# Optimization experiments

Hardware: AMD Instinct MI355X
Metric: run time of the kernel (lower is better)

## Reference

```python
import jax, jax.numpy as jnp
import numpy as np

N = 196608   # total bonds in batch
H = 256      # hidden_size
NH = 8       # num_heads
D = H // NH  # att_size = 32
S = 4096     # num molecules (segments)
EPS = 1e-5


def setup_inputs() -> dict:
    key = jax.random.key(0)
    ks = jax.random.split(key, 12)
    f32 = jnp.float32
    return {
        "message": jax.random.normal(ks[0], (N, H), f32),
        "W_q": jax.random.normal(ks[1], (H, H), f32) * 0.05,
        "W_k": jax.random.normal(ks[2], (H, H), f32) * 0.05,
        "W_v": jax.random.normal(ks[3], (H, H), f32) * 0.05,
        "W_r": jax.random.normal(ks[4], (D, D), f32) * 0.15,
        "w_alpha": jax.random.normal(ks[5], (D,), f32),
        "w_beta": jax.random.normal(ks[6], (D,), f32),
        "W_o": jax.random.normal(ks[7], (H, H), f32) * 0.05,
        "b_o": jax.random.normal(ks[8], (H,), f32) * 0.02,
        "gamma": 1.0 + 0.1 * jax.random.normal(ks[9], (H,), f32),
        "beta_ln": 0.1 * jax.random.normal(ks[10], (H,), f32),
        "segment_ids": jnp.sort(jax.random.randint(ks[11], (N,), 0, S, dtype=jnp.int32)),
        "num_segments": S,
    }


def reference(message, W_q, W_k, W_v, W_r, w_alpha, w_beta, W_o, b_o,
              gamma, beta_ln, segment_ids, num_segments):
    scale = D ** (-0.5)
    # projections (torch Linear: y = x @ W.T), split heads -> [N, NH, D]
    q = (message @ W_q.T).reshape(-1, NH, D)
    k = (message @ W_k.T).reshape(-1, NH, D)
    v = (message @ W_v.T).reshape(-1, NH, D)
    # additive attention: softmax over feature dim d (per bond, per head)
    alpha = jax.nn.softmax(q * w_alpha * scale, axis=-1)
    # global query: sum over bonds within each molecule -> [S, NH, D]
    gq = jax.ops.segment_sum(alpha * q, segment_ids, num_segments=num_segments)
    p = gq[segment_ids] * k                      # [N, NH, D]
    beta = jax.nn.softmax(p * w_beta * scale, axis=-1)
    gk = jax.ops.segment_sum(beta * p, segment_ids, num_segments=num_segments)
    kvi = gk[segment_ids] * v                    # key-value interaction [N, NH, D]
    out = jnp.einsum('nhd,ed->nhe', kvi, W_r) + q  # weight_r on d, residual with q
    out = jax.nn.relu(out)                       # chemprop ReLU activation; dropout p=0
    out = out.reshape(-1, NH * D)
    out = out @ W_o.T + b_o
    # LayerNorm over hidden dim
    mu = jnp.mean(out, axis=-1, keepdims=True)
    var = jnp.mean(jnp.square(out - mu), axis=-1, keepdims=True)
    out = (out - mu) * jax.lax.rsqrt(var + EPS) * gamma + beta_ln
    # prepend cached zero vector (padding row), as the torch loop does for i == 0
    zero = jnp.zeros((1, H), dtype=out.dtype)
    return jnp.concatenate([zero, out], axis=0)
```

## Files before the change

### kernel.cpp

```cpp
#include <hip/hip_runtime.h>
#include <hip/hip_bf16.h>

#define N_BONDS 196608
#define HID     256
#define NSEG    4096
#define SMSCALE 0.17677669529663687f
#define LN_EPS  1e-5f
#define CHUNK   64

typedef __hip_bfloat16 bf16;
typedef __attribute__((ext_vector_type(8))) short short8_t;
typedef __attribute__((ext_vector_type(4))) float f32x4_t;

__device__ __forceinline__ float bf2f(bf16 x) { return __bfloat162float(x); }
__device__ __forceinline__ short f2bs(float f) {
    union { bf16 b; short s; } cv; cv.b = __float2bfloat16(f); return cv.s;
}
__device__ __forceinline__ float us2f(ushort u) {
    union { ushort u; bf16 b; } cv; cv.u = u; return __bfloat162float(cv.b);
}

__device__ __forceinline__ float gmax32(float x) {
#pragma unroll
    for (int m = 16; m >= 1; m >>= 1) x = fmaxf(x, __shfl_xor(x, m));
    return x;
}
__device__ __forceinline__ float gsum32(float x) {
#pragma unroll
    for (int m = 16; m >= 1; m >>= 1) x += __shfl_xor(x, m);
    return x;
}

__global__ void cast_kernel(const float* __restrict__ src, ushort* __restrict__ dst, int n4) {
    int i = blockIdx.x * blockDim.x + threadIdx.x;
    const int stride = gridDim.x * blockDim.x;
    for (; i < n4; i += stride) {
        float4 v = reinterpret_cast<const float4*>(src)[i];
        union { ushort4 u; bf16 b[4]; } cv;
        cv.b[0] = __float2bfloat16(v.x);
        cv.b[1] = __float2bfloat16(v.y);
        cv.b[2] = __float2bfloat16(v.z);
        cv.b[3] = __float2bfloat16(v.w);
        reinterpret_cast<ushort4*>(dst)[i] = cv.u;
    }
}

template <typename OutT>
__global__ __launch_bounds__(256, 2) void gemm_bt(const ushort* __restrict__ A,
                                                  const ushort* __restrict__ W,
                                                  OutT* __restrict__ C) {
    __shared__ __align__(16) char lds[128 * 512];
    const int t = threadIdx.x;
    const int colhalf = blockIdx.y;
#pragma unroll
    for (int it = 0; it < 16; ++it) {
        int c = it * 256 + t;
        int j = c >> 5, kc = c & 31;
        uint4 val = *reinterpret_cast<const uint4*>(W + ((colhalf << 7) + j) * HID + (kc << 3));
        *reinterpret_cast<uint4*>(lds + j * 512 + ((kc << 4) ^ ((j & 7) << 4))) = val;
    }
    __syncthreads();

    const int wave = t >> 6, lane = t & 63;
    const int lr = lane & 15, lk = lane >> 4;
    const long rowbase = (long)blockIdx.x * 128 + wave * 32;

    f32x4_t acc[2][8];
#pragma unroll
    for (int r = 0; r < 2; ++r)
#pragma unroll
        for (int cc = 0; cc < 8; ++cc) acc[r][cc] = (f32x4_t){0.f, 0.f, 0.f, 0.f};

    const ushort* a0 = A + (rowbase + lr) * HID;
    const ushort* a1 = a0 + 16 * HID;
#pragma unroll
    for (int k0 = 0; k0 < HID; k0 += 32) {
        const int koff = k0 + lk * 8;
        short8_t af0 = *reinterpret_cast<const short8_t*>(a0 + koff);
        short8_t af1 = *reinterpret_cast<const short8_t*>(a1 + koff);
#pragma unroll
        for (int cc = 0; cc < 8; ++cc) {
            const int j = cc * 16 + lr;
            short8_t bfr = *reinterpret_cast<const short8_t*>(
                lds + j * 512 + (((k0 << 1) + (lk << 4)) ^ ((j & 7) << 4)));
            acc[0][cc] = __builtin_amdgcn_mfma_f32_16x16x32_bf16(af0, bfr, acc[0][cc], 0, 0, 0);
            acc[1][cc] = __builtin_amdgcn_mfma_f32_16x16x32_bf16(af1, bfr, acc[1][cc], 0, 0, 0);
        }
    }
#pragma unroll
    for (int r = 0; r < 2; ++r) {
#pragma unroll
        for (int cc = 0; cc < 8; ++cc) {
            const int col = (colhalf << 7) + cc * 16 + lr;
#pragma unroll
            for (int reg = 0; reg < 4; ++reg) {
                const long row = rowbase + r * 16 + lk * 4 + reg;
                const float v = acc[r][cc][reg];
                if constexpr (sizeof(OutT) == 2) C[row * HID + col] = __float2bfloat16(v);
                else                             C[row * HID + col] = v;
            }
        }
    }
}

__global__ __launch_bounds__(256) void alpha_gq_kernel(const bf16* __restrict__ qb,
                                                       const float* __restrict__ w_alpha,
                                                       const int* __restrict__ seg,
                                                       float* __restrict__ gq) {
    const int j = threadIdx.x;
    const float wa = w_alpha[j & 31] * SMSCALE;
    const long n0 = (long)blockIdx.x * CHUNK;
    float acc = 0.f;
    int cur = -1;
    for (int i = 0; i < CHUNK; ++i) {
        const long n = n0 + i;
        const int s = seg[n];
        const float qv = bf2f(qb[n * HID + j]);
        const float x = qv * wa;
        const float m = gmax32(x);
        const float e = __expf(x - m);
        const float ssum = gsum32(e);
        const float alpha = e / ssum;
        if (s != cur) {
            if (cur >= 0) atomicAdd(&gq[(long)cur * HID + j], acc);
            acc = 0.f;
            cur = s;
        }
        acc += alpha * qv;
    }
    atomicAdd(&gq[(long)cur * HID + j], acc);
}

__global__ __launch_bounds__(256) void beta_gk_kernel(const bf16* __restrict__ kb,
                                                      const float* __restrict__ gq,
                                                      const float* __restrict__ w_beta,
                                                      const int* __restrict__ seg,
                                                      float* __restrict__ gk) {
    const int j = threadIdx.x;
    const float wb = w_beta[j & 31] * SMSCALE;
    const long n0 = (long)blockIdx.x * CHUNK;
    float acc = 0.f;
    int cur = -1;
    for (int i = 0; i < CHUNK; ++i) {
        const long n = n0 + i;
        const int s = seg[n];
        const float kv = bf2f(kb[n * HID + j]);
        const float p = gq[(long)s * HID + j] * kv;
        const float x = p * wb;
        const float m = gmax32(x);
        const float e = __expf(x - m);
        const float ssum = gsum32(e);
        const float beta = e / ssum;
        if (s != cur) {
            if (cur >= 0) atomicAdd(&gk[(long)cur * HID + j], acc);
            acc = 0.f;
            cur = s;
        }
        acc += beta * p;
    }
    atomicAdd(&gk[(long)cur * HID + j], acc);
}

__global__ __launch_bounds__(256) void act_exact_kernel(const ushort* __restrict__ vb,
                                                        const ushort* __restrict__ qb,
                                                        const float* __restrict__ gk,
                                                        const float* __restrict__ Wr,
                                                        const int* __restrict__ seg,
                                                        ushort* __restrict__ act) {
    __shared__ __align__(16) float wr_lds[1024];
    const int t = threadIdx.x;
#pragma unroll
    for (int i = 0; i < 4; ++i) wr_lds[i * 256 + t] = Wr[i * 256 + t];
    __syncthreads();

    const long tid = (long)blockIdx.x * 256 + t;
    const int n = (int)(tid >> 3), h = (int)(tid & 7);
    const int sid = seg[n];

    const float* gp = gk + (long)sid * HID + h * 32;
    const ushort* vp = vb + tid * 32;
    float kvi[32];
#pragma unroll
    for (int dq = 0; dq < 4; ++dq) {
        short8_t v8 = *reinterpret_cast<const short8_t*>(vp + dq * 8);
        float4 ga = reinterpret_cast<const float4*>(gp)[dq * 2];
        float4 gb = reinterpret_cast<const float4*>(gp)[dq * 2 + 1];
        kvi[dq * 8 + 0] = ga.x * us2f((ushort)v8[0]);
        kvi[dq * 8 + 1] = ga.y * us2f((ushort)v8[1]);
        kvi[dq * 8 + 2] = ga.z * us2f((ushort)v8[2]);
        kvi[dq * 8 + 3] = ga.w * us2f((ushort)v8[3]);
        kvi[dq * 8 + 4] = gb.x * us2f((ushort)v8[4]);
        kvi[dq * 8 + 5] = gb.y * us2f((ushort)v8[5]);
        kvi[dq * 8 + 6] = gb.z * us2f((ushort)v8[6]);
        kvi[dq * 8 + 7] = gb.w * us2f((ushort)v8[7]);
    }

    const ushort* qp = qb + tid * 32;
    short8_t q8[4];
#pragma unroll
    for (int i = 0; i < 4; ++i) q8[i] = *reinterpret_cast<const short8_t*>(qp + i * 8);

    short8_t ob[4];
#pragma unroll
    for (int e = 0; e < 32; ++e) {
        float acc = 0.f;
        const float4* wre = reinterpret_cast<const float4*>(wr_lds + e * 32);
#pragma unroll
        for (int dq = 0; dq < 8; ++dq) {
            float4 w = wre[dq];
            acc = fmaf(kvi[dq * 4 + 0], w.x, acc);
            acc = fmaf(kvi[dq * 4 + 1], w.y, acc);
            acc = fmaf(kvi[dq * 4 + 2], w.z, acc);
            acc = fmaf(kvi[dq * 4 + 3], w.w, acc);
        }
        const float qv = us2f((ushort)q8[e >> 3][e & 7]);
        ob[e >> 3][e & 7] = f2bs(fmaxf(acc + qv, 0.f));
    }

    ushort* ap = act + tid * 32;
#pragma unroll
    for (int i = 0; i < 4; ++i) *reinterpret_cast<short8_t*>(ap + i * 8) = ob[i];
}

__global__ __launch_bounds__(256) void ln_kernel(const float* __restrict__ tmp,
                                                 const float* __restrict__ b_o,
                                                 const float* __restrict__ gamma,
                                                 const float* __restrict__ beta_ln,
                                                 float* __restrict__ out) {
    const int wave = threadIdx.x >> 6, lane = threadIdx.x & 63;
    const long row = (long)blockIdx.x * 4 + wave;
    const float4 bo = reinterpret_cast<const float4*>(b_o)[lane];
    const float4 g = reinterpret_cast<const float4*>(gamma)[lane];
    const float4 bl = reinterpret_cast<const float4*>(beta_ln)[lane];
    float4 x = reinterpret_cast<const float4*>(tmp + row * HID)[lane];
    x.x += bo.x; x.y += bo.y; x.z += bo.z; x.w += bo.w;
    float s = x.x + x.y + x.z + x.w;
#pragma unroll
    for (int m = 32; m >= 1; m >>= 1) s += __shfl_xor(s, m);
    const float mu = s * (1.f / HID);
    float4 dx = {x.x - mu, x.y - mu, x.z - mu, x.w - mu};
    float sq = dx.x * dx.x + dx.y * dx.y + dx.z * dx.z + dx.w * dx.w;
#pragma unroll
    for (int m = 32; m >= 1; m >>= 1) sq += __shfl_xor(sq, m);
    const float r = rsqrtf(sq * (1.f / HID) + LN_EPS);
    float4 o;
    o.x = dx.x * r * g.x + bl.x;
    o.y = dx.y * r * g.y + bl.y;
    o.z = dx.z * r * g.z + bl.z;
    o.w = dx.w * r * g.w + bl.w;
    reinterpret_cast<float4*>(out + (row + 1) * HID)[lane] = o;
}

extern "C" void kernel_launch(void* const* d_in, const int* in_sizes, int n_in,
                              void* d_out, int out_size, void* d_ws, size_t ws_size,
                              hipStream_t stream) {
    const float* msg    = (const float*)d_in[0];
    const float* Wq     = (const float*)d_in[1];
    const float* Wk     = (const float*)d_in[2];
    const float* Wv     = (const float*)d_in[3];
    const float* Wr     = (const float*)d_in[4];
    const float* walpha = (const float*)d_in[5];
    const float* wbeta  = (const float*)d_in[6];
    const float* Wo     = (const float*)d_in[7];
    const float* bo     = (const float*)d_in[8];
    const float* gamma  = (const float*)d_in[9];
    const float* betaln = (const float*)d_in[10];
    const int*   seg    = (const int*)d_in[11];

    char* ws = (char*)d_ws;
    const size_t nh = (size_t)N_BONDS * HID;
    size_t off = 0;
    bf16* msgb = (bf16*)(ws + off); off += nh * 2;
    bf16* qb   = (bf16*)(ws + off); off += nh * 2;
    bf16* kb   = (bf16*)(ws + off); off += nh * 2;
    bf16* vb   = (bf16*)(ws + off); off += nh * 2;
    bf16* wqb  = (bf16*)(ws + off); off += (size_t)HID * HID * 2;
    bf16* wkb  = (bf16*)(ws + off); off += (size_t)HID * HID * 2;
    bf16* wvb  = (bf16*)(ws + off); off += (size_t)HID * HID * 2;
    bf16* wob  = (bf16*)(ws + off); off += (size_t)HID * HID * 2;
    float* gq  = (float*)(ws + off); off += (size_t)NSEG * HID * 4;
    float* gk  = (float*)(ws + off); off += (size_t)NSEG * HID * 4;
    bf16*  act = msgb;
    float* tmp = (float*)qb;

    hipMemsetAsync(gq, 0, (size_t)2 * NSEG * HID * 4, stream);
    hipMemsetAsync(d_out, 0, HID * sizeof(float), stream);

    cast_kernel<<<4096, 256, 0, stream>>>(msg, (ushort*)msgb, (int)(nh / 4));
    cast_kernel<<<64, 256, 0, stream>>>(Wq, (ushort*)wqb, HID * HID / 4);
    cast_kernel<<<64, 256, 0, stream>>>(Wk, (ushort*)wkb, HID * HID / 4);
    cast_kernel<<<64, 256, 0, stream>>>(Wv, (ushort*)wvb, HID * HID / 4);
    cast_kernel<<<64, 256, 0, stream>>>(Wo, (ushort*)wob, HID * HID / 4);

    dim3 gg(N_BONDS / 128, 2);
    gemm_bt<bf16><<<gg, 256, 0, stream>>>((const ushort*)msgb, (const ushort*)wqb, qb);
    gemm_bt<bf16><<<gg, 256, 0, stream>>>((const ushort*)msgb, (const ushort*)wkb, kb);
    gemm_bt<bf16><<<gg, 256, 0, stream>>>((const ushort*)msgb, (const ushort*)wvb, vb);

    alpha_gq_kernel<<<N_BONDS / CHUNK, 256, 0, stream>>>(qb, walpha, seg, gq);
    beta_gk_kernel<<<N_BONDS / CHUNK, 256, 0, stream>>>(kb, gq, wbeta, seg, gk);

    act_exact_kernel<<<N_BONDS * 8 / 256, 256, 0, stream>>>((const ushort*)vb, (const ushort*)qb,
                                                            gk, Wr, seg, (ushort*)act);

    gemm_bt<float><<<gg, 256, 0, stream>>>((const ushort*)act, (const ushort*)wob, tmp);
    ln_kernel<<<N_BONDS / 4, 256, 0, stream>>>(tmp, bo, gamma, betaln, (float*)d_out);
}
```

Before: 716.0 us.

## Remap softmax-segment kernels to one thread per (bond, head) with register softmax

The alpha/gq and beta/gk kernels move from one thread per feature element, which used cross-lane shuffles for each softmax, to one thread per bond-head pair. Each thread loads 32 bf16 values with vector loads and does the max/exp/sum in registers. Each thread now walks 12 consecutive bonds and flushes its 32-wide accumulator with atomics at segment boundaries. It also caches the gq row in registers while the segment is unchanged. This removes shuffle reductions and scalar loads, but raises register pressure, makes loads strided across lanes (each lane reads 64 contiguous bytes) and adds more atomics per segment boundary.

```diff
diff --git a/kernel.cpp b/kernel.cpp
--- a/kernel.cpp
+++ b/kernel.cpp
@@ -6,29 +6,17 @@
 #define NSEG    4096
 #define SMSCALE 0.17677669529663687f
 #define LN_EPS  1e-5f
-#define CHUNK   64
+#define SB      12
 
 typedef __hip_bfloat16 bf16;
 typedef __attribute__((ext_vector_type(8))) short short8_t;
 typedef __attribute__((ext_vector_type(4))) float f32x4_t;
 
-__device__ __forceinline__ float bf2f(bf16 x) { return __bfloat162float(x); }
 __device__ __forceinline__ short f2bs(float f) {
     union { bf16 b; short s; } cv; cv.b = __float2bfloat16(f); return cv.s;
 }
 __device__ __forceinline__ float us2f(ushort u) {
     union { ushort u; bf16 b; } cv; cv.u = u; return __bfloat162float(cv.b);
-}
-
-__device__ __forceinline__ float gmax32(float x) {
-#pragma unroll
-    for (int m = 16; m >= 1; m >>= 1) x = fmaxf(x, __shfl_xor(x, m));
-    return x;
-}
-__device__ __forceinline__ float gsum32(float x) {
-#pragma unroll
-    for (int m = 16; m >= 1; m >>= 1) x += __shfl_xor(x, m);
-    return x;
 }
 
 __global__ void cast_kernel(const float* __restrict__ src, ushort* __restrict__ dst, int n4) {
@@ -103,62 +91,122 @@
     }
 }
 
-__global__ __launch_bounds__(256) void alpha_gq_kernel(const bf16* __restrict__ qb,
+__global__ __launch_bounds__(256) void alpha_gq_kernel(const ushort* __restrict__ qb,
                                                        const float* __restrict__ w_alpha,
                                                        const int* __restrict__ seg,
                                                        float* __restrict__ gq) {
-    const int j = threadIdx.x;
-    const float wa = w_alpha[j & 31] * SMSCALE;
-    const long n0 = (long)blockIdx.x * CHUNK;
-    float acc = 0.f;
-    int cur = -1;
-    for (int i = 0; i < CHUNK; ++i) {
-        const long n = n0 + i;
+    const int t = threadIdx.x;
+    const int h = t & 7, c = t >> 3;
+    const long nbase = (long)blockIdx.x * (32 * SB) + (long)c * SB;
+
+    float wa[32];
+#pragma unroll
+    for (int d = 0; d < 32; ++d) wa[d] = w_alpha[d] * SMSCALE;
+
+    float acc[32];
+#pragma unroll
+    for (int d = 0; d < 32; ++d) acc[d] = 0.f;
+    int cur = seg[nbase];
+
+    for (int i = 0; i < SB; ++i) {
+        const long n = nbase + i;
         const int s = seg[n];
-        const float qv = bf2f(qb[n * HID + j]);
-        const float x = qv * wa;
-        const float m = gmax32(x);
-        const float e = __expf(x - m);
-        const float ssum = gsum32(e);
-        const float alpha = e / ssum;
+        const ushort* qp = qb + n * HID + h * 32;
+        float q[32];
+#pragma unroll
+        for (int v = 0; v < 4; ++v) {
+            short8_t q8 = *reinterpret_cast<const short8_t*>(qp + v * 8);
+#pragma unroll
+            for (int e = 0; e < 8; ++e) q[v * 8 + e] = us2f((ushort)q8[e]);
+        }
+        float x[32];
+        float m = -1e30f;
+#pragma unroll
+        for (int d = 0; d < 32; ++d) { x[d] = q[d] * wa[d]; m = fmaxf(m, x[d]); }
+        float ssum = 0.f;
+#pragma unroll
+        for (int d = 0; d < 32; ++d) { x[d] = __expf(x[d] - m); ssum += x[d]; }
+        const float inv = 1.f / ssum;
         if (s != cur) {
-            if (cur >= 0) atomicAdd(&gq[(long)cur * HID + j], acc);
-            acc = 0.f;
+            float* gp = gq + (long)cur * HID + h * 32;
+#pragma unroll
+            for (int d = 0; d < 32; ++d) { atomicAdd(gp + d, acc[d]); acc[d] = 0.f; }
             cur = s;
         }
-        acc += alpha * qv;
-    }
-    atomicAdd(&gq[(long)cur * HID + j], acc);
-}
-
-__global__ __launch_bounds__(256) void beta_gk_kernel(const bf16* __restrict__ kb,
+#pragma unroll
+        for (int d = 0; d < 32; ++d) acc[d] = fmaf(x[d] * inv, q[d], acc[d]);
+    }
+    float* gp = gq + (long)cur * HID + h * 32;
+#pragma unroll
+    for (int d = 0; d < 32; ++d) atomicAdd(gp + d, acc[d]);
+}
+
+__global__ __launch_bounds__(256) void beta_gk_kernel(const ushort* __restrict__ kb,
                                                       const float* __restrict__ gq,
                                                       const float* __restrict__ w_beta,
                                                       const int* __restrict__ seg,
                                                       float* __restrict__ gk) {
-    const int j = threadIdx.x;
-    const float wb = w_beta[j & 31] * SMSCALE;
-    const long n0 = (long)blockIdx.x * CHUNK;
-    float acc = 0.f;
-    int cur = -1;
-    for (int i = 0; i < CHUNK; ++i) {
-        const long n = n0 + i;
+    const int t = threadIdx.x;
+    const int h = t & 7, c = t >> 3;
+    const long nbase = (long)blockIdx.x * (32 * SB) + (long)c * SB;
+
+    float wb[32];
+#pragma unroll
+    for (int d = 0; d < 32; ++d) wb[d] = w_beta[d] * SMSCALE;
+
+    float acc[32];
+#pragma unroll
+    for (int d = 0; d < 32; ++d) acc[d] = 0.f;
+    int cur = seg[nbase];
+    float gqr[32];
+    {
+        const float* gp = gq + (long)cur * HID + h * 32;
+#pragma unroll
+        for (int v = 0; v < 8; ++v) {
+            float4 g4 = reinterpret_cast<const float4*>(gp)[v];
+            gqr[v * 4 + 0] = g4.x; gqr[v * 4 + 1] = g4.y;
+            gqr[v * 4 + 2] = g4.z; gqr[v * 4 + 3] = g4.w;
+        }
+    }
+
+    for (int i = 0; i < SB; ++i) {
+        const long n = nbase + i;
         const int s = seg[n];
-        const float kv = bf2f(kb[n * HID + j]);
-        const float p = gq[(long)s * HID + j] * kv;
-        const float x = p * wb;
-        const float m = gmax32(x);
-        const float e = __expf(x - m);
-        const float ssum = gsum32(e);
-        const float beta = e / ssum;
         if (s != cur) {
-            if (cur >= 0) atomicAdd(&gk[(long)cur * HID + j], acc);
-            acc = 0.f;
+            float* gpk = gk + (long)cur * HID + h * 32;
+#pragma unroll
+            for (int d = 0; d < 32; ++d) { atomicAdd(gpk + d, acc[d]); acc[d] = 0.f; }
             cur = s;
-        }
-        acc += beta * p;
-    }
-    atomicAdd(&gk[(long)cur * HID + j], acc);
+            const float* gp = gq + (long)cur * HID + h * 32;
+#pragma unroll
+            for (int v = 0; v < 8; ++v) {
+                float4 g4 = reinterpret_cast<const float4*>(gp)[v];
+                gqr[v * 4 + 0] = g4.x; gqr[v * 4 + 1] = g4.y;
+                gqr[v * 4 + 2] = g4.z; gqr[v * 4 + 3] = g4.w;
+            }
+        }
+        const ushort* kp = kb + n * HID + h * 32;
+        float p[32];
+#pragma unroll
+        for (int v = 0; v < 4; ++v) {
+            short8_t k8 = *reinterpret_cast<const short8_t*>(kp + v * 8);
+#pragma unroll
+            for (int e = 0; e < 8; ++e) p[v * 8 + e] = gqr[v * 8 + e] * us2f((ushort)k8[e]);
+        }
+        float x[32];
+        float m = -1e30f;
+#pragma unroll
+        for (int d = 0; d < 32; ++d) { x[d] = p[d] * wb[d]; m = fmaxf(m, x[d]); }
+        float ssum = 0.f;
+#pragma unroll
+        for (int d = 0; d < 32; ++d) { x[d] = __expf(x[d] - m); ssum += x[d]; }
+        const float inv = 1.f / ssum;
+#pragma unroll
+        for (int d = 0; d < 32; ++d) acc[d] = fmaf(x[d] * inv, p[d], acc[d]);
+    }
+    float* gpk = gk + (long)cur * HID + h * 32;
+#pragma unroll
+    for (int d = 0; d < 32; ++d) atomicAdd(gpk + d, acc[d]);
 }
 
 __global__ __launch_bounds__(256) void act_exact_kernel(const ushort* __restrict__ vb,
@@ -297,8 +345,8 @@
     gemm_bt<bf16><<<gg, 256, 0, stream>>>((const ushort*)msgb, (const ushort*)wkb, kb);
     gemm_bt<bf16><<<gg, 256, 0, stream>>>((const ushort*)msgb, (const ushort*)wvb, vb);
 
-    alpha_gq_kernel<<<N_BONDS / CHUNK, 256, 0, stream>>>(qb, walpha, seg, gq);
-    beta_gk_kernel<<<N_BONDS / CHUNK, 256, 0, stream>>>(kb, gq, wbeta, seg, gk);
+    alpha_gq_kernel<<<N_BONDS / (32 * SB), 256, 0, stream>>>((const ushort*)qb, walpha, seg, gq);
+    beta_gk_kernel<<<N_BONDS / (32 * SB), 256, 0, stream>>>((const ushort*)kb, gq, wbeta, seg, gk);
 
     act_exact_kernel<<<N_BONDS * 8 / 256, 256, 0, stream>>>((const ushort*)vb, (const ushort*)qb,
                                                             gk, Wr, seg, (ushort*)act);
```

Measured after the change: 1.102 ms. +53.8%, slower.
